# Performance work log

Hardware: AMD Instinct MI355X
Metric: run time of the kernel (lower is better)

The kernel has to match this reference:

```python
import jax, jax.numpy as jnp
import numpy as np


def setup_inputs() -> dict:
    key = jax.random.key(0)
    k1, k2, k3, k4 = jax.random.split(key, 4)
    B, N, D, d_dir = 2, 512, 512, 64
    scale_in = 1.0 / np.sqrt(D)
    scale_dir = 1.0 / np.sqrt(d_dir)
    t = jax.random.normal(k1, (B, N, D), dtype=jnp.float32)
    Wq = jax.random.normal(k2, (d_dir, D), dtype=jnp.float32) * scale_in
    Wk = jax.random.normal(k3, (d_dir, D), dtype=jnp.float32) * scale_in
    Wv = jax.random.normal(k4, (D, d_dir), dtype=jnp.float32) * scale_dir
    return {"t": t, "Wq": Wq, "Wk": Wk, "Wv": Wv}


def reference(t, Wq, Wk, Wv):
    # t: (B, N, D); Wq, Wk: (d_dir, D); Wv: (D, d_dir)
    q = jnp.einsum('bnd,ed->bne', t, Wq)  # (B, N, d_dir)
    k = jnp.einsum('bnd,ed->bne', t, Wk)  # (B, N, d_dir)
    had = q[:, :, None, :] * k[:, None, :, :]  # (B, N, N, d_dir)
    kappa = jnp.einsum('bije,de->bijd', had, Wv)  # (B, N, N, D)
    return kappa
```

## Files before the change

kernel.cpp:

```cpp
#include <hip/hip_runtime.h>
#include <hip/hip_bf16.h>

#define NB   512
#define DB   512
#define EB   64
#define JT   16
#define TPB  16

typedef __bf16 bf16x8 __attribute__((ext_vector_type(8)));
typedef float  f32x4  __attribute__((ext_vector_type(4)));

__global__ __launch_bounds__(64) void qk_proj_bf16(
    const float* __restrict__ t,
    const float* __restrict__ Wq,
    const float* __restrict__ Wk,
    const float* __restrict__ Wv,
    __bf16* __restrict__ qb,
    __bf16* __restrict__ kb,
    __bf16* __restrict__ wvb)
{
    __shared__ float trow[DB];
    const int bn = blockIdx.x;
    const int e  = threadIdx.x;

    if (bn < DB)
        wvb[bn * EB + e] = (__bf16)Wv[bn * EB + e];

    #pragma unroll
    for (int idx = 0; idx < DB / 64; ++idx)
        trow[idx * 64 + e] = t[(size_t)bn * DB + idx * 64 + e];
    __syncthreads();

    float aq = 0.f, ak = 0.f;
    const float* wqr = Wq + (size_t)e * DB;
    const float* wkr = Wk + (size_t)e * DB;
    #pragma unroll 8
    for (int d = 0; d < DB; ++d) {
        const float tv = trow[d];
        aq += tv * wqr[d];
        ak += tv * wkr[d];
    }
    qb[bn * EB + e] = (__bf16)aq;
    kb[bn * EB + e] = (__bf16)ak;
}

__global__ __launch_bounds__(256) void kappa_mfma(
    const __bf16* __restrict__ qb,
    const __bf16* __restrict__ kb,
    const __bf16* __restrict__ wvb,
    float* __restrict__ out)
{
    const int blk = blockIdx.x;
    const int bi  = blk >> 1;
    const int b   = bi >> 9;
    const int jt0 = (blk & 1) * TPB;
    const int w    = threadIdx.x >> 6;
    const int l    = threadIdx.x & 63;
    const int lrow = l & 15;
    const int lgrp = l >> 4;
    const int dbase = w * 128;

    __shared__ float lds[4 * JT * 128];
    float* __restrict__ wtile = lds + w * (JT * 128);

    const bf16x8 qv0 = *reinterpret_cast<const bf16x8*>(qb + (size_t)bi * EB + lgrp * 8);
    const bf16x8 qv1 = *reinterpret_cast<const bf16x8*>(qb + (size_t)bi * EB + 32 + lgrp * 8);

    bf16x8 bfrag[8][2];
    #pragma unroll
    for (int df = 0; df < 8; ++df) {
        const int d = dbase + df * 16 + lrow;
        #pragma unroll
        for (int ks = 0; ks < 2; ++ks) {
            const bf16x8 wv = *reinterpret_cast<const bf16x8*>(
                wvb + (size_t)d * EB + ks * 32 + lgrp * 8);
            const bf16x8 qq = ks ? qv1 : qv0;
            bf16x8 f;
            #pragma unroll
            for (int x = 0; x < 8; ++x)
                f[x] = (__bf16)((float)wv[x] * (float)qq[x]);
            bfrag[df][ks] = f;
        }
    }

    const __bf16* __restrict__ kbase = kb + (size_t)b * NB * EB;

    bf16x8 kv0 = *reinterpret_cast<const bf16x8*>(kbase + (size_t)(jt0 * JT + lrow) * EB + lgrp * 8);
    bf16x8 kv1 = *reinterpret_cast<const bf16x8*>(kbase + (size_t)(jt0 * JT + lrow) * EB + 32 + lgrp * 8);

    const int r_lo = l >> 5;
    const int cc   = l & 31;

    for (int t = 0; t < TPB; ++t) {
        f32x4 acc[8];
        #pragma unroll
        for (int df = 0; df < 8; ++df) {
            acc[df] = (f32x4){0.f, 0.f, 0.f, 0.f};
            acc[df] = __builtin_amdgcn_mfma_f32_16x16x32_bf16(bfrag[df][0], kv0, acc[df], 0, 0, 0);
            acc[df] = __builtin_amdgcn_mfma_f32_16x16x32_bf16(bfrag[df][1], kv1, acc[df], 0, 0, 0);
        }

        if (t + 1 < TPB) {
            const int jn = (jt0 + t + 1) * JT + lrow;
            kv0 = *reinterpret_cast<const bf16x8*>(kbase + (size_t)jn * EB + lgrp * 8);
            kv1 = *reinterpret_cast<const bf16x8*>(kbase + (size_t)jn * EB + 32 + lgrp * 8);
        }

        asm volatile("" ::: "memory");
        #pragma unroll
        for (int df = 0; df < 8; ++df) {
            const int sc = (df * 4 + lgrp) ^ (lrow & 7);
            *reinterpret_cast<f32x4*>(wtile + lrow * 128 + sc * 4) = acc[df];
        }
        asm volatile("" ::: "memory");

        float* __restrict__ obase =
            out + ((size_t)bi * NB + (size_t)(jt0 + t) * JT) * DB + dbase;
        #pragma unroll
        for (int p = 0; p < 8; ++p) {
            const int r  = 2 * p + r_lo;
            const int sc = cc ^ (r & 7);
            const f32x4 v = *reinterpret_cast<const f32x4*>(wtile + r * 128 + sc * 4);
            __builtin_nontemporal_store(
                v, reinterpret_cast<f32x4*>(obase + (size_t)r * DB + cc * 4));
        }
    }
}

extern "C" void kernel_launch(void* const* d_in, const int* in_sizes, int n_in,
                              void* d_out, int out_size, void* d_ws, size_t ws_size,
                              hipStream_t stream) {
    const float* t  = (const float*)d_in[0];
    const float* Wq = (const float*)d_in[1];
    const float* Wk = (const float*)d_in[2];
    const float* Wv = (const float*)d_in[3];
    float* out = (float*)d_out;

    const int B = 2;

    __bf16* qb  = (__bf16*)d_ws;
    __bf16* kbf = qb + (size_t)B * NB * EB;
    __bf16* wvb = kbf + (size_t)B * NB * EB;

    qk_proj_bf16<<<dim3(B * NB), dim3(64), 0, stream>>>(t, Wq, Wk, Wv, qb, kbf, wvb);

    kappa_mfma<<<dim3(2048), dim3(256), 0, stream>>>(qb, kbf, wvb, out);
}
```

Measured before the change: 241.4 us.

## Double-buffer LDS output tiles, use regular stores, and process two rows per projection block

```diff
diff --git a/kernel.cpp b/kernel.cpp
--- a/kernel.cpp
+++ b/kernel.cpp
@@ -19,29 +19,30 @@
     __bf16* __restrict__ kb,
     __bf16* __restrict__ wvb)
 {
-    __shared__ float trow[DB];
-    const int bn = blockIdx.x;
-    const int e  = threadIdx.x;
+    const int blk = blockIdx.x;
+    const int bn0 = blk * 2;
+    const int e   = threadIdx.x;
 
-    if (bn < DB)
-        wvb[bn * EB + e] = (__bf16)Wv[bn * EB + e];
+    wvb[blk * EB + e] = (__bf16)Wv[blk * EB + e];
 
-    #pragma unroll
-    for (int idx = 0; idx < DB / 64; ++idx)
-        trow[idx * 64 + e] = t[(size_t)bn * DB + idx * 64 + e];
-    __syncthreads();
-
-    float aq = 0.f, ak = 0.f;
-    const float* wqr = Wq + (size_t)e * DB;
-    const float* wkr = Wk + (size_t)e * DB;
+    float aq0 = 0.f, ak0 = 0.f, aq1 = 0.f, ak1 = 0.f;
+    const float* __restrict__ wqr = Wq + (size_t)e * DB;
+    const float* __restrict__ wkr = Wk + (size_t)e * DB;
+    const float* __restrict__ t0  = t + (size_t)bn0 * DB;
+    const float* __restrict__ t1  = t0 + DB;
     #pragma unroll 8
     for (int d = 0; d < DB; ++d) {
-        const float tv = trow[d];
-        aq += tv * wqr[d];
-        ak += tv * wkr[d];
+        const float wqv = wqr[d];
+        const float wkv = wkr[d];
+        const float tv0 = t0[d];
+        const float tv1 = t1[d];
+        aq0 += tv0 * wqv;  ak0 += tv0 * wkv;
+        aq1 += tv1 * wqv;  ak1 += tv1 * wkv;
     }
-    qb[bn * EB + e] = (__bf16)aq;
-    kb[bn * EB + e] = (__bf16)ak;
+    qb[(size_t)bn0 * EB + e]       = (__bf16)aq0;
+    kb[(size_t)bn0 * EB + e]       = (__bf16)ak0;
+    qb[(size_t)(bn0 + 1) * EB + e] = (__bf16)aq1;
+    kb[(size_t)(bn0 + 1) * EB + e] = (__bf16)ak1;
 }
 
 __global__ __launch_bounds__(256) void kappa_mfma(
@@ -60,8 +61,9 @@
     const int lgrp = l >> 4;
     const int dbase = w * 128;
 
-    __shared__ float lds[4 * JT * 128];
-    float* __restrict__ wtile = lds + w * (JT * 128);
+    __shared__ float lds[2 * 4 * JT * 128];
+    float* __restrict__ wtA = lds + w * (JT * 128);
+    float* __restrict__ wtB = lds + 4 * JT * 128 + w * (JT * 128);
 
     const bf16x8 qv0 = *reinterpret_cast<const bf16x8*>(qb + (size_t)bi * EB + lgrp * 8);
     const bf16x8 qv1 = *reinterpret_cast<const bf16x8*>(qb + (size_t)bi * EB + 32 + lgrp * 8);
@@ -91,38 +93,76 @@
     const int r_lo = l >> 5;
     const int cc   = l & 31;
 
-    for (int t = 0; t < TPB; ++t) {
-        f32x4 acc[8];
-        #pragma unroll
-        for (int df = 0; df < 8; ++df) {
-            acc[df] = (f32x4){0.f, 0.f, 0.f, 0.f};
-            acc[df] = __builtin_amdgcn_mfma_f32_16x16x32_bf16(bfrag[df][0], kv0, acc[df], 0, 0, 0);
-            acc[df] = __builtin_amdgcn_mfma_f32_16x16x32_bf16(bfrag[df][1], kv1, acc[df], 0, 0, 0);
+    for (int t2 = 0; t2 < TPB; t2 += 2) {
+        {
+            f32x4 acc[8];
+            #pragma unroll
+            for (int df = 0; df < 8; ++df) {
+                acc[df] = (f32x4){0.f, 0.f, 0.f, 0.f};
+                acc[df] = __builtin_amdgcn_mfma_f32_16x16x32_bf16(bfrag[df][0], kv0, acc[df], 0, 0, 0);
+                acc[df] = __builtin_amdgcn_mfma_f32_16x16x32_bf16(bfrag[df][1], kv1, acc[df], 0, 0, 0);
+            }
+            {
+                const int jn = (jt0 + t2 + 1) * JT + lrow;
+                kv0 = *reinterpret_cast<const bf16x8*>(kbase + (size_t)jn * EB + lgrp * 8);
+                kv1 = *reinterpret_cast<const bf16x8*>(kbase + (size_t)jn * EB + 32 + lgrp * 8);
+            }
+            asm volatile("" ::: "memory");
+            #pragma unroll
+            for (int df = 0; df < 8; ++df) {
+                const int sc = (df * 4 + lgrp) ^ (lrow & 7);
+                *reinterpret_cast<f32x4*>(wtA + lrow * 128 + sc * 4) = acc[df];
+            }
+            asm volatile("" ::: "memory");
+            f32x4 ve[8];
+            #pragma unroll
+            for (int p = 0; p < 8; ++p) {
+                const int r  = 2 * p + r_lo;
+                const int sc = cc ^ (r & 7);
+                ve[p] = *reinterpret_cast<const f32x4*>(wtA + r * 128 + sc * 4);
+            }
+            float* __restrict__ obase =
+                out + ((size_t)bi * NB + (size_t)(jt0 + t2) * JT) * DB + dbase;
+            #pragma unroll
+            for (int p = 0; p < 8; ++p) {
+                const int r = 2 * p + r_lo;
+                *reinterpret_cast<f32x4*>(obase + (size_t)r * DB + cc * 4) = ve[p];
+            }
         }
-
-        if (t + 1 < TPB) {
-            const int jn = (jt0 + t + 1) * JT + lrow;
-            kv0 = *reinterpret_cast<const bf16x8*>(kbase + (size_t)jn * EB + lgrp * 8);
-            kv1 = *reinterpret_cast<const bf16x8*>(kbase + (size_t)jn * EB + 32 + lgrp * 8);
-        }
-
-        asm volatile("" ::: "memory");
-        #pragma unroll
-        for (int df = 0; df < 8; ++df) {
-            const int sc = (df * 4 + lgrp) ^ (lrow & 7);
-            *reinterpret_cast<f32x4*>(wtile + lrow * 128 + sc * 4) = acc[df];
-        }
-        asm volatile("" ::: "memory");
-
-        float* __restrict__ obase =
-            out + ((size_t)bi * NB + (size_t)(jt0 + t) * JT) * DB + dbase;
-        #pragma unroll
-        for (int p = 0; p < 8; ++p) {
-            const int r  = 2 * p + r_lo;
-            const int sc = cc ^ (r & 7);
-            const f32x4 v = *reinterpret_cast<const f32x4*>(wtile + r * 128 + sc * 4);
-            __builtin_nontemporal_store(
-                v, reinterpret_cast<f32x4*>(obase + (size_t)r * DB + cc * 4));
+        {
+            f32x4 acc[8];
+            #pragma unroll
+            for (int df = 0; df < 8; ++df) {
+                acc[df] = (f32x4){0.f, 0.f, 0.f, 0.f};
+                acc[df] = __builtin_amdgcn_mfma_f32_16x16x32_bf16(bfrag[df][0], kv0, acc[df], 0, 0, 0);
+                acc[df] = __builtin_amdgcn_mfma_f32_16x16x32_bf16(bfrag[df][1], kv1, acc[df], 0, 0, 0);
+            }
+            if (t2 + 2 < TPB) {
+                const int jn = (jt0 + t2 + 2) * JT + lrow;
+                kv0 = *reinterpret_cast<const bf16x8*>(kbase + (size_t)jn * EB + lgrp * 8);
+                kv1 = *reinterpret_cast<const bf16x8*>(kbase + (size_t)jn * EB + 32 + lgrp * 8);
+            }
+            asm volatile("" ::: "memory");
+            #pragma unroll
+            for (int df = 0; df < 8; ++df) {
+                const int sc = (df * 4 + lgrp) ^ (lrow & 7);
+                *reinterpret_cast<f32x4*>(wtB + lrow * 128 + sc * 4) = acc[df];
+            }
+            asm volatile("" ::: "memory");
+            f32x4 vo[8];
+            #pragma unroll
+            for (int p = 0; p < 8; ++p) {
+                const int r  = 2 * p + r_lo;
+                const int sc = cc ^ (r & 7);
+                vo[p] = *reinterpret_cast<const f32x4*>(wtB + r * 128 + sc * 4);
+            }
+            float* __restrict__ obase =
+                out + ((size_t)bi * NB + (size_t)(jt0 + t2 + 1) * JT) * DB + dbase;
+            #pragma unroll
+            for (int p = 0; p < 8; ++p) {
+                const int r = 2 * p + r_lo;
+                *reinterpret_cast<f32x4*>(obase + (size_t)r * DB + cc * 4) = vo[p];
+            }
         }
     }
 }
@@ -142,7 +182,7 @@
     __bf16* kbf = qb + (size_t)B * NB * EB;
     __bf16* wvb = kbf + (size_t)B * NB * EB;
 
-    qk_proj_bf16<<<dim3(B * NB), dim3(64), 0, stream>>>(t, Wq, Wk, Wv, qb, kbf, wvb);
+    qk_proj_bf16<<<dim3(512), dim3(64), 0, stream>>>(t, Wq, Wk, Wv, qb, kbf, wvb);
 
     kappa_mfma<<<dim3(2048), dim3(256), 0, stream>>>(qb, kbf, wvb, out);
 }
```

Measured after the change: 219.9 us. -8.9%, faster.
